# Kernel tuning notes

Measured on AMD Instinct MI355X. Metric: run time of the kernel, lower is better.

## Reference

```python
import jax, jax.numpy as jnp
import numpy as np

N_EMBD = 1024
N_HEAD = 16
HEAD_SIZE = N_EMBD // N_HEAD
EPS = 1e-5


def layer_norm(x, gamma, beta):
    mu = jnp.mean(x, axis=-1, keepdims=True)
    var = jnp.var(x, axis=-1, keepdims=True)
    return (x - mu) * jax.lax.rsqrt(var + EPS) * gamma + beta


def setup_inputs() -> dict:
    key = jax.random.key(0)
    ks = jax.random.split(key, 12)
    B, T, C, H, hs = 2, 2048, N_EMBD, N_HEAD, HEAD_SIZE
    s = lambda fan_in: 1.0 / np.sqrt(fan_in)
    return {
        "x": jax.random.normal(ks[0], (B, T, C), dtype=jnp.float32),
        "Wq": jax.random.normal(ks[1], (H, C, hs), dtype=jnp.float32) * s(C),
        "Wk": jax.random.normal(ks[2], (H, C, hs), dtype=jnp.float32) * s(C),
        "Wv": jax.random.normal(ks[3], (H, C, hs), dtype=jnp.float32) * s(C),
        "Wproj": jax.random.normal(ks[4], (C, C), dtype=jnp.float32) * s(C),
        "bproj": jax.random.normal(ks[5], (C,), dtype=jnp.float32) * 0.01,
        "g1": jnp.ones((C,), dtype=jnp.float32),
        "b1": jnp.zeros((C,), dtype=jnp.float32),
        "g2": jnp.ones((C,), dtype=jnp.float32),
        "b2": jnp.zeros((C,), dtype=jnp.float32),
        "W_ff1": jax.random.normal(ks[6], (C, 4 * C), dtype=jnp.float32) * s(C),
        "b_ff1": jax.random.normal(ks[7], (4 * C,), dtype=jnp.float32) * 0.01,
        "W_ff2": jax.random.normal(ks[8], (4 * C, C), dtype=jnp.float32) * s(4 * C),
        "b_ff2": jax.random.normal(ks[9], (C,), dtype=jnp.float32) * 0.01,
    }


def reference(x, Wq, Wk, Wv, Wproj, bproj, g1, b1, g2, b2, W_ff1, b_ff1, W_ff2, b_ff2):
    B, T, C = x.shape
    # --- LN1 + multi-head causal self-attention ---
    h = layer_norm(x, g1, b1)
    q = jnp.einsum("btc,hcd->bhtd", h, Wq)  # [B,H,T,hs]
    k = jnp.einsum("btc,hcd->bhtd", h, Wk)
    v = jnp.einsum("btc,hcd->bhtd", h, Wv)
    scale = HEAD_SIZE ** -0.5
    wei = jnp.einsum("bhtd,bhsd->bhts", q, k) * scale  # [B,H,T,T]
    mask = jnp.tril(jnp.ones((T, T), dtype=bool))
    wei = jnp.where(mask, wei, -jnp.inf)
    wei = jax.nn.softmax(wei, axis=-1)
    out = jnp.einsum("bhts,bhsd->bhtd", wei, v)  # [B,H,T,hs]
    out = out.transpose(0, 2, 1, 3).reshape(B, T, C)  # concat heads
    sa = out @ Wproj + bproj
    x = x + sa
    # --- LN2 + FFN ---
    h2 = layer_norm(x, g2, b2)
    ff = jax.nn.relu(h2 @ W_ff1 + b_ff1) @ W_ff2 + b_ff2
    return x + ff
```

## Files before the change

kernel.cpp:

```cpp
#include <hip/hip_runtime.h>
#include <hip/hip_bf16.h>

#define N_EMBD 1024
#define N_HEAD 16
#define HEADSZ 64
#define BATCH  2
#define SEQ    2048
#define ROWS   (BATCH*SEQ)

typedef __attribute__((ext_vector_type(8))) short bf16x8;
typedef __attribute__((ext_vector_type(4))) float f32x4;

__device__ __forceinline__ short f2bs(float v){
    union { __hip_bfloat16 b; short s; } u; u.b = __float2bfloat16(v); return u.s;
}
__device__ __forceinline__ short scale8th(short s){
    union { unsigned i; float f; } u; u.i = ((unsigned)(unsigned short)s) << 16;
    return f2bs(u.f * 0.125f);
}
__device__ __forceinline__ void gload16(const short* g, short* l){
    __builtin_amdgcn_global_load_lds(
        (const __attribute__((address_space(1))) unsigned int*)g,
        (__attribute__((address_space(3))) unsigned int*)l, 16, 0, 0);
}

__global__ __launch_bounds__(256) void tr_cvt(const float* __restrict__ in,
                                              short* __restrict__ out,
                                              int R, int Cc,
                                              size_t in_z, size_t out_z)
{
    __shared__ float t[32][33];
    const int tx = threadIdx.x & 31, ty = threadIdx.x >> 5;
    const int j0 = blockIdx.x * 32, i0 = blockIdx.y * 32;
    const float* ip = in + (size_t)blockIdx.z * in_z;
    short* op = out + (size_t)blockIdx.z * out_z;
#pragma unroll
    for (int p = 0; p < 4; ++p)
        t[ty + p * 8][tx] = ip[(size_t)(i0 + ty + p * 8) * Cc + j0 + tx];
    __syncthreads();
#pragma unroll
    for (int p = 0; p < 4; ++p)
        op[(size_t)(j0 + ty + p * 8) * R + i0 + tx] = f2bs(t[tx][ty + p * 8]);
}

__global__ __launch_bounds__(256) void tr3_cvt(const float* __restrict__ Wq,
                                               const float* __restrict__ Wk,
                                               const float* __restrict__ Wv,
                                               short* __restrict__ w2t)
{
    __shared__ float t[32][33];
    const int tx = threadIdx.x & 31, ty = threadIdx.x >> 5;
    const int which = blockIdx.z >> 4, head = blockIdx.z & 15;
    const int j0 = blockIdx.x * 32, i0 = blockIdx.y * 32;
    const float* ip = (which == 0 ? Wq : which == 1 ? Wk : Wv) + (size_t)head * 65536;
    short* op = w2t + (size_t)which * 1048576 + (size_t)head * 65536;
#pragma unroll
    for (int p = 0; p < 4; ++p)
        t[ty + p * 8][tx] = ip[(size_t)(i0 + ty + p * 8) * 64 + j0 + tx];
    __syncthreads();
#pragma unroll
    for (int p = 0; p < 4; ++p)
        op[(size_t)(j0 + ty + p * 8) * 1024 + i0 + tx] = f2bs(t[tx][ty + p * 8]);
}

__global__ __launch_bounds__(256) void vt_tr(const short* __restrict__ qkv,
                                             short* __restrict__ vt)
{
    __shared__ short t[64][65];
    const int tid = threadIdx.x;
    const int sr = tid >> 2, sc = (tid & 3) * 16;
    const int col0 = blockIdx.x * 64, tok0 = blockIdx.y * 64;
    const short* ip = qkv + (size_t)(tok0 + sr) * 3072 + 2048 + col0 + sc;
    bf16x8 v0 = *(const bf16x8*)ip;
    bf16x8 v1 = *(const bf16x8*)(ip + 8);
#pragma unroll
    for (int i = 0; i < 8; ++i) { t[sr][sc + i] = v0[i]; t[sr][sc + 8 + i] = v1[i]; }
    __syncthreads();
    bf16x8 a, bq;
#pragma unroll
    for (int i = 0; i < 8; ++i) { a[i] = t[sc + i][sr]; bq[i] = t[sc + 8 + i][sr]; }
    short* op = vt + (size_t)(col0 + sr) * 4096 + tok0 + sc;
    *(bf16x8*)op = a;
    *(bf16x8*)(op + 8) = bq;
}

__global__ __launch_bounds__(256) void ln_k(const float* __restrict__ x,
                                            const float* __restrict__ g,
                                            const float* __restrict__ bta,
                                            short* __restrict__ out)
{
    const int row = blockIdx.x;
    const int tid = threadIdx.x;
    const float* xr = x + (size_t)row * N_EMBD;
    float4 v = *(const float4*)(xr + tid * 4);
    float s  = v.x + v.y + v.z + v.w;
    float s2 = v.x * v.x + v.y * v.y + v.z * v.z + v.w * v.w;
#pragma unroll
    for (int off = 32; off; off >>= 1) {
        s  += __shfl_xor(s,  off, 64);
        s2 += __shfl_xor(s2, off, 64);
    }
    __shared__ float rs[4], rs2[4];
    const int wave = tid >> 6, lane = tid & 63;
    if (lane == 0) { rs[wave] = s; rs2[wave] = s2; }
    __syncthreads();
    s  = rs[0] + rs[1] + rs[2] + rs[3];
    s2 = rs2[0] + rs2[1] + rs2[2] + rs2[3];
    const float mean = s * (1.f / N_EMBD);
    const float var  = s2 * (1.f / N_EMBD) - mean * mean;
    const float rsig = rsqrtf(var + 1e-5f);
    float4 gv = *(const float4*)(g + tid * 4);
    float4 bv = *(const float4*)(bta + tid * 4);
    short4 o;
    o.x = f2bs((v.x - mean) * rsig * gv.x + bv.x);
    o.y = f2bs((v.y - mean) * rsig * gv.y + bv.y);
    o.z = f2bs((v.z - mean) * rsig * gv.z + bv.z);
    o.w = f2bs((v.w - mean) * rsig * gv.w + bv.w);
    *(short4*)(out + (size_t)row * N_EMBD + tid * 4) = o;
}

__global__ __launch_bounds__(256) void pln_fin(const float* __restrict__ p0,
                                               const float* __restrict__ p1,
                                               const float* __restrict__ bias,
                                               const float* __restrict__ x,
                                               const float* __restrict__ g,
                                               const float* __restrict__ bta,
                                               float* __restrict__ x2,
                                               short* __restrict__ h2)
{
    const int row = blockIdx.x, tid = threadIdx.x;
    const size_t base = (size_t)row * N_EMBD + tid * 4;
    float4 a  = *(const float4*)(p0 + base);
    float4 c  = *(const float4*)(p1 + base);
    float4 xx = *(const float4*)(x + base);
    float4 bb = *(const float4*)(bias + tid * 4);
    float4 v;
    v.x = a.x + c.x + xx.x + bb.x;
    v.y = a.y + c.y + xx.y + bb.y;
    v.z = a.z + c.z + xx.z + bb.z;
    v.w = a.w + c.w + xx.w + bb.w;
    *(float4*)(x2 + base) = v;
    float s  = v.x + v.y + v.z + v.w;
    float s2 = v.x * v.x + v.y * v.y + v.z * v.z + v.w * v.w;
#pragma unroll
    for (int off = 32; off; off >>= 1) {
        s  += __shfl_xor(s,  off, 64);
        s2 += __shfl_xor(s2, off, 64);
    }
    __shared__ float rs[4], rs2[4];
    const int wave = tid >> 6, lane = tid & 63;
    if (lane == 0) { rs[wave] = s; rs2[wave] = s2; }
    __syncthreads();
    s  = rs[0] + rs[1] + rs[2] + rs[3];
    s2 = rs2[0] + rs2[1] + rs2[2] + rs2[3];
    const float mean = s * (1.f / N_EMBD);
    const float var  = s2 * (1.f / N_EMBD) - mean * mean;
    const float rsig = rsqrtf(var + 1e-5f);
    float4 gv = *(const float4*)(g + tid * 4);
    float4 bv = *(const float4*)(bta + tid * 4);
    short4 o;
    o.x = f2bs((v.x - mean) * rsig * gv.x + bv.x);
    o.y = f2bs((v.y - mean) * rsig * gv.y + bv.y);
    o.z = f2bs((v.z - mean) * rsig * gv.z + bv.z);
    o.w = f2bs((v.w - mean) * rsig * gv.w + bv.w);
    *(short4*)(h2 + base) = o;
}

__global__ __launch_bounds__(256) void mfma_gemm(
    const short* __restrict__ A,
    const short* __restrict__ Bt,
    const float* __restrict__ bias,
    const float* __restrict__ resid,
    float* __restrict__ outf,
    float* __restrict__ outf2,
    short* __restrict__ outb,
    int M, int N, int K, int kz, int relu)
{
    __shared__ __align__(16) short As[3][128 * 32];
    __shared__ __align__(16) short Bs[3][128 * 32];
    const int tid  = threadIdx.x;
    const int lane = tid & 63, w = tid >> 6;
    const int quad = lane >> 4, l16 = lane & 15;
    const int row0 = blockIdx.y * 128, col0 = blockIdx.x * 128;
    const int wm = (w >> 1) * 64, wn = (w & 1) * 64;
    const int koff = blockIdx.z * kz;
    const int kend = kz ? kz : K;
    const int nk   = kend >> 5;

    f32x4 acc[4][4];
#pragma unroll
    for (int i = 0; i < 4; ++i)
#pragma unroll
        for (int j = 0; j < 4; ++j)
            acc[i][j] = f32x4{0.f, 0.f, 0.f, 0.f};

    const int c0  = w * 128 + lane;
    const int c1  = c0 + 64;
    const int ar0 = c0 >> 2, ak0 = (((c0 & 3) ^ ((ar0 >> 1) & 3))) * 8;
    const int ar1 = c1 >> 2, ak1 = (((c1 & 3) ^ ((ar1 >> 1) & 3))) * 8;
    const short* aG0 = A  + (size_t)(row0 + ar0) * K + koff + ak0;
    const short* aG1 = A  + (size_t)(row0 + ar1) * K + koff + ak1;
    const short* bG0 = Bt + (size_t)(col0 + ar0) * K + koff + ak0;
    const short* bG1 = Bt + (size_t)(col0 + ar1) * K + koff + ak1;
    const int lofs = w * 1024;

    const int gsw = (quad ^ ((l16 >> 1) & 3)) * 8;

    gload16(aG0, As[0] + lofs);
    gload16(aG1, As[0] + lofs + 512);
    gload16(bG0, Bs[0] + lofs);
    gload16(bG1, Bs[0] + lofs + 512);
    if (nk > 1) {
        gload16(aG0 + 32, As[1] + lofs);
        gload16(aG1 + 32, As[1] + lofs + 512);
        gload16(bG0 + 32, Bs[1] + lofs);
        gload16(bG1 + 32, Bs[1] + lofs + 512);
    }

    for (int k = 0; k < nk; ++k) {
        if (k + 1 < nk) asm volatile("s_waitcnt vmcnt(4)" ::: "memory");
        else            asm volatile("s_waitcnt vmcnt(0)" ::: "memory");
        __builtin_amdgcn_s_barrier();
        if (k + 2 < nk) {
            const int nb = (k + 2) % 3;
            const int ko = (k + 2) * 32;
            gload16(aG0 + ko, As[nb] + lofs);
            gload16(aG1 + ko, As[nb] + lofs + 512);
            gload16(bG0 + ko, Bs[nb] + lofs);
            gload16(bG1 + ko, Bs[nb] + lofs + 512);
        }
        const int cur = k % 3;

        bf16x8 af[4], bfr[4];
#pragma unroll
        for (int i = 0; i < 4; ++i)
            af[i]  = *(const bf16x8*)(As[cur] + (wm + i * 16 + l16) * 32 + gsw);
#pragma unroll
        for (int j = 0; j < 4; ++j)
            bfr[j] = *(const bf16x8*)(Bs[cur] + (wn + j * 16 + l16) * 32 + gsw);
#pragma unroll
        for (int i = 0; i < 4; ++i)
#pragma unroll
            for (int j = 0; j < 4; ++j)
                acc[i][j] = __builtin_amdgcn_mfma_f32_16x16x32_bf16(
                    af[i], bfr[j], acc[i][j], 0, 0, 0);
    }

    float* of = blockIdx.z ? outf2 : outf;
#pragma unroll
    for (int i = 0; i < 4; ++i) {
        const int rbase = row0 + wm + i * 16 + quad * 4;
#pragma unroll
        for (int j = 0; j < 4; ++j) {
            const int c = col0 + wn + j * 16 + l16;
            const float bv = bias ? bias[c] : 0.f;
#pragma unroll
            for (int r = 0; r < 4; ++r) {
                float v = acc[i][j][r] + bv;
                if (relu) v = fmaxf(v, 0.f);
                const size_t idx = (size_t)(rbase + r) * N + c;
                if (resid) v += resid[idx];
                if (outb) outb[idx] = f2bs(v);
                else      of[idx] = v;
            }
        }
    }
}

__global__ __launch_bounds__(256) void mfma_gemm64(
    const short* __restrict__ A,
    const short* __restrict__ Bt,
    float* __restrict__ outf,
    float* __restrict__ outf2,
    int K, int kz)
{
    __shared__ __align__(16) short As[3][64 * 32];
    __shared__ __align__(16) short Bs[3][128 * 32];
    const int tid  = threadIdx.x;
    const int lane = tid & 63, w = tid >> 6;
    const int quad = lane >> 4, l16 = lane & 15;
    const int lin  = (int)blockIdx.y * 8 + (int)blockIdx.x;
    const int swz  = (lin & 7) * 64 + (lin >> 3);
    const int col0 = (swz & 7) * 128;
    const int row0 = (swz >> 3) * 64;
    const int wr = w >> 1, wc = w & 1;
    const int koff = blockIdx.z * kz;
    const int nk   = kz >> 5;

    f32x4 acc[2][4];
#pragma unroll
    for (int i = 0; i < 2; ++i)
#pragma unroll
        for (int j = 0; j < 4; ++j)
            acc[i][j] = f32x4{0.f, 0.f, 0.f, 0.f};

    const int ia  = w * 64 + lane;
    const int ar  = ia >> 2;
    const int aak = ((ia & 3) ^ ((ar >> 1) & 3)) * 8;
    const short* aG = A + (size_t)(row0 + ar) * K + koff + aak;
    const int aofs = w * 512;
    const int c0  = w * 128 + lane;
    const int c1  = c0 + 64;
    const int br0 = c0 >> 2, bk0 = ((c0 & 3) ^ ((br0 >> 1) & 3)) * 8;
    const int br1 = c1 >> 2, bk1 = ((c1 & 3) ^ ((br1 >> 1) & 3)) * 8;
    const short* bG0 = Bt + (size_t)(col0 + br0) * K + koff + bk0;
    const short* bG1 = Bt + (size_t)(col0 + br1) * K + koff + bk1;
    const int bofs = w * 1024;

    const int gsw = (quad ^ ((l16 >> 1) & 3)) * 8;

    gload16(aG, As[0] + aofs);
    gload16(bG0, Bs[0] + bofs);
    gload16(bG1, Bs[0] + bofs + 512);
    if (nk > 1) {
        gload16(aG + 32, As[1] + aofs);
        gload16(bG0 + 32, Bs[1] + bofs);
        gload16(bG1 + 32, Bs[1] + bofs + 512);
    }

    for (int k = 0; k < nk; ++k) {
        if (k + 1 < nk) asm volatile("s_waitcnt vmcnt(3)" ::: "memory");
        else            asm volatile("s_waitcnt vmcnt(0)" ::: "memory");
        __builtin_amdgcn_s_barrier();
        if (k + 2 < nk) {
            const int nb = (k + 2) % 3;
            const int ko = (k + 2) * 32;
            gload16(aG + ko, As[nb] + aofs);
            gload16(bG0 + ko, Bs[nb] + bofs);
            gload16(bG1 + ko, Bs[nb] + bofs + 512);
        }
        const int cur = k % 3;

        bf16x8 af[2], bfr[4];
#pragma unroll
        for (int i = 0; i < 2; ++i)
            af[i]  = *(const bf16x8*)(As[cur] + (wr * 32 + i * 16 + l16) * 32 + gsw);
#pragma unroll
        for (int j = 0; j < 4; ++j)
            bfr[j] = *(const bf16x8*)(Bs[cur] + (wc * 64 + j * 16 + l16) * 32 + gsw);
#pragma unroll
        for (int i = 0; i < 2; ++i)
#pragma unroll
            for (int j = 0; j < 4; ++j)
                acc[i][j] = __builtin_amdgcn_mfma_f32_16x16x32_bf16(
                    af[i], bfr[j], acc[i][j], 0, 0, 0);
    }

    float* of = blockIdx.z ? outf2 : outf;
#pragma unroll
    for (int i = 0; i < 2; ++i) {
        const int rbase = row0 + wr * 32 + i * 16 + quad * 4;
#pragma unroll
        for (int j = 0; j < 4; ++j) {
            const int c = col0 + wc * 64 + j * 16 + l16;
#pragma unroll
            for (int r = 0; r < 4; ++r)
                of[(size_t)(rbase + r) * 1024 + c] = acc[i][j][r];
        }
    }
}

__global__ __launch_bounds__(256) void ff2_fin(const float* __restrict__ p0,
                                               const float* __restrict__ bias,
                                               const float* __restrict__ x2,
                                               float* __restrict__ out)
{
    const size_t i = ((size_t)blockIdx.x * 256 + threadIdx.x) * 4;
    float4 a = *(const float4*)(p0 + i);
    float4 b = *(const float4*)(out + i);
    float4 r = *(const float4*)(x2 + i);
    float4 bb = *(const float4*)(bias + (i & 1023));
    float4 o;
    o.x = a.x + b.x + r.x + bb.x;
    o.y = a.y + b.y + r.y + bb.y;
    o.z = a.z + b.z + r.z + bb.z;
    o.w = a.w + b.w + r.w + bb.w;
    *(float4*)(out + i) = o;
}

__global__ __launch_bounds__(256) void attn_k(const short* __restrict__ qkv,
                                              const short* __restrict__ vt,
                                              short* __restrict__ att)
{
    __shared__ __align__(16) short Ks[2][64 * 64];
    __shared__ __align__(16) short Vs[2][64 * 64];
    __shared__ __align__(16) short Ps[64 * 64];
    const int tid  = threadIdx.x;
    const int lane = tid & 63, w = tid >> 6;
    const int quad = lane >> 4, l16 = lane & 15;
    const int bh = blockIdx.y, b = bh >> 4, head = bh & 15;

    const int srow = lane >> 3;
    const int sw   = ((lane & 7) ^ srow) * 8;
    const int cidx = (quad ^ (l16 & 7)) * 8;

    const int k4 = (bh >> 3) & 3;
    int qt = (k4 & 2) ? ((int)blockIdx.x ^ 16) : (int)blockIdx.x;
    if (k4 & 1) qt = 31 - qt;
    const int t0 = qt * 64;
    const int ntiles = qt + 1;

    const short* qp = qkv + (size_t)(b * SEQ + t0 + w * 16 + l16) * 3072
                      + head * 64 + quad * 8;
    bf16x8 qf0 = *(const bf16x8*)qp;
    bf16x8 qf1 = *(const bf16x8*)(qp + 32);
#pragma unroll
    for (int i = 0; i < 8; ++i) { qf0[i] = scale8th(qf0[i]); qf1[i] = scale8th(qf1[i]); }

    float mrow = -INFINITY, lrow = 0.f;
    f32x4 O[4];
#pragma unroll
    for (int jn = 0; jn < 4; ++jn) O[jn] = f32x4{0.f, 0.f, 0.f, 0.f};

    {
        const short* kg = qkv + (size_t)(b * SEQ + w * 16 + srow) * 3072
                          + 1024 + head * 64 + sw;
        const short* vg = vt + (size_t)(head * 64 + w * 16 + srow) * 4096
                          + b * SEQ + sw;
        short* kL = Ks[0] + w * 1024;
        short* vL = Vs[0] + w * 1024;
        gload16(kg, kL); gload16(kg + (size_t)8 * 3072, kL + 512);
        gload16(vg, vL); gload16(vg + (size_t)8 * 4096, vL + 512);
    }

    for (int kt = 0; kt < ntiles; ++kt) {
        const int cur = kt & 1;
        asm volatile("s_waitcnt vmcnt(0) lgkmcnt(0)\n\ts_barrier" ::: "memory");
        if (kt + 1 < ntiles) {
            const int s1 = (kt + 1) * 64;
            const short* kg = qkv + (size_t)(b * SEQ + s1 + w * 16 + srow) * 3072
                              + 1024 + head * 64 + sw;
            const short* vg = vt + (size_t)(head * 64 + w * 16 + srow) * 4096
                              + b * SEQ + s1 + sw;
            short* kL = Ks[cur ^ 1] + w * 1024;
            short* vL = Vs[cur ^ 1] + w * 1024;
            gload16(kg, kL); gload16(kg + (size_t)8 * 3072, kL + 512);
            gload16(vg, vL); gload16(vg + (size_t)8 * 4096, vL + 512);
        }

        f32x4 S[4];
        const short* Kb = Ks[cur];
#pragma unroll
        for (int jn = 0; jn < 4; ++jn) {
            S[jn] = f32x4{0.f, 0.f, 0.f, 0.f};
            const short* kp = Kb + (jn * 16 + l16) * 64;
            bf16x8 b0 = *(const bf16x8*)(kp + cidx);
            bf16x8 b1 = *(const bf16x8*)(kp + (cidx ^ 32));
            S[jn] = __builtin_amdgcn_mfma_f32_16x16x32_bf16(b0, qf0, S[jn], 0, 0, 0);
            S[jn] = __builtin_amdgcn_mfma_f32_16x16x32_bf16(b1, qf1, S[jn], 0, 0, 0);
        }

        float Sv[4][4];
        const int qrow = t0 + w * 16 + l16;
        const int s0 = kt * 64;
#pragma unroll
        for (int jn = 0; jn < 4; ++jn)
#pragma unroll
            for (int r = 0; r < 4; ++r)
                Sv[jn][r] = S[jn][r];
        if (kt == ntiles - 1) {
#pragma unroll
            for (int jn = 0; jn < 4; ++jn)
#pragma unroll
                for (int r = 0; r < 4; ++r)
                    if (s0 + jn * 16 + quad * 4 + r > qrow) Sv[jn][r] = -INFINITY;
        }
        float tmx[4];
#pragma unroll
        for (int jn = 0; jn < 4; ++jn)
            tmx[jn] = fmaxf(fmaxf(Sv[jn][0], Sv[jn][1]), fmaxf(Sv[jn][2], Sv[jn][3]));
        float pm = fmaxf(fmaxf(tmx[0], tmx[1]), fmaxf(tmx[2], tmx[3]));
        pm = fmaxf(pm, __shfl_xor(pm, 16, 64));
        pm = fmaxf(pm, __shfl_xor(pm, 32, 64));
        const float mn    = fmaxf(mrow, pm);
        const float alpha = __expf(mrow - mn);
#pragma unroll
        for (int jn = 0; jn < 4; ++jn)
#pragma unroll
            for (int r = 0; r < 4; ++r)
                Sv[jn][r] = __expf(Sv[jn][r] - mn);
        float tsm[4];
#pragma unroll
        for (int jn = 0; jn < 4; ++jn)
            tsm[jn] = (Sv[jn][0] + Sv[jn][1]) + (Sv[jn][2] + Sv[jn][3]);
        float ps = (tsm[0] + tsm[1]) + (tsm[2] + tsm[3]);
        ps += __shfl_xor(ps, 16, 64);
        ps += __shfl_xor(ps, 32, 64);
        lrow = lrow * alpha + ps;
        mrow = mn;
#pragma unroll
        for (int r = 0; r < 4; ++r) {
            const float a = __shfl(alpha, quad * 4 + r, 64);
#pragma unroll
            for (int jn = 0; jn < 4; ++jn) O[jn][r] *= a;
        }

#pragma unroll
        for (int jn = 0; jn < 4; ++jn) {
            short4 pv;
            pv.x = f2bs(Sv[jn][0]); pv.y = f2bs(Sv[jn][1]);
            pv.z = f2bs(Sv[jn][2]); pv.w = f2bs(Sv[jn][3]);
            const int prow = w * 16 + l16;
            const int pcol = jn * 16 + quad * 4;
            const int chunk = (pcol >> 3) ^ (l16 & 7);
            *(short4*)(Ps + prow * 64 + chunk * 8 + (pcol & 7)) = pv;
        }
        asm volatile("s_waitcnt lgkmcnt(0)" ::: "memory");

        const short* pp = Ps + (w * 16 + l16) * 64;
        bf16x8 pf0 = *(const bf16x8*)(pp + cidx);
        bf16x8 pf1 = *(const bf16x8*)(pp + (cidx ^ 32));
        const short* Vb = Vs[cur];
#pragma unroll
        for (int jn = 0; jn < 4; ++jn) {
            const short* vp = Vb + (jn * 16 + l16) * 64;
            bf16x8 v0 = *(const bf16x8*)(vp + cidx);
            bf16x8 v1 = *(const bf16x8*)(vp + (cidx ^ 32));
            O[jn] = __builtin_amdgcn_mfma_f32_16x16x32_bf16(pf0, v0, O[jn], 0, 0, 0);
            O[jn] = __builtin_amdgcn_mfma_f32_16x16x32_bf16(pf1, v1, O[jn], 0, 0, 0);
        }
    }

#pragma unroll
    for (int r = 0; r < 4; ++r) {
        const float lr  = __shfl(lrow, quad * 4 + r, 64);
        const float inv = 1.f / lr;
        const size_t rowoff = (size_t)(b * SEQ + t0 + w * 16 + quad * 4 + r) * N_EMBD
                              + head * 64 + l16;
#pragma unroll
        for (int jn = 0; jn < 4; ++jn)
            att[rowoff + jn * 16] = f2bs(O[jn][r] * inv);
    }
}

extern "C" void kernel_launch(void* const* d_in, const int* in_sizes, int n_in,
                              void* d_out, int out_size, void* d_ws, size_t ws_size,
                              hipStream_t stream)
{
    const float* x     = (const float*)d_in[0];
    const float* Wq    = (const float*)d_in[1];
    const float* Wk    = (const float*)d_in[2];
    const float* Wv    = (const float*)d_in[3];
    const float* Wproj = (const float*)d_in[4];
    const float* bproj = (const float*)d_in[5];
    const float* g1    = (const float*)d_in[6];
    const float* b1    = (const float*)d_in[7];
    const float* g2    = (const float*)d_in[8];
    const float* b2    = (const float*)d_in[9];
    const float* Wff1  = (const float*)d_in[10];
    const float* bff1  = (const float*)d_in[11];
    const float* Wff2  = (const float*)d_in[12];
    const float* bff2  = (const float*)d_in[13];
    float* out = (float*)d_out;

    char* ws = (char*)d_ws;
    short* w2t  = (short*)(ws + 0);
    short* wpt  = (short*)(ws + 6291456);
    short* wf1t = (short*)(ws + 8388608);
    short* wf2t = (short*)(ws + 16777216);
    short* h    = (short*)(ws + 25165824);
    short* qkv  = (short*)(ws + 33554432);
    short* vt   = (short*)(ws + 58720256);
    short* att  = (short*)(ws + 67108864);
    float* x2   = (float*)(ws + 75497472);
    short* h2   = h;
    float* p0p  = (float*)(ws + 33554432);
    float* p1p  = (float*)(ws + 50331648);
    short* ff   = qkv;
    float* p0f  = (float*)(ws + 0);

    tr3_cvt<<<dim3(2, 32, 48),  256, 0, stream>>>(Wq, Wk, Wv, w2t);
    tr_cvt<<<dim3(32, 32, 1),  256, 0, stream>>>(Wproj, wpt,  1024, 1024, 0, 0);
    tr_cvt<<<dim3(128, 32, 1), 256, 0, stream>>>(Wff1, wf1t,  1024, 4096, 0, 0);
    tr_cvt<<<dim3(32, 128, 1), 256, 0, stream>>>(Wff2, wf2t,  4096, 1024, 0, 0);

    ln_k<<<ROWS, 256, 0, stream>>>(x, g1, b1, h);
    mfma_gemm<<<dim3(3072 / 128, ROWS / 128), 256, 0, stream>>>(
        h, w2t, nullptr, nullptr, nullptr, nullptr, qkv, ROWS, 3072, N_EMBD, 0, 0);
    vt_tr<<<dim3(16, 64), 256, 0, stream>>>(qkv, vt);
    attn_k<<<dim3(32, BATCH * N_HEAD), 256, 0, stream>>>(qkv, vt, att);
    mfma_gemm64<<<dim3(8, 64, 2), 256, 0, stream>>>(att, wpt, p0p, p1p, N_EMBD, 512);
    pln_fin<<<ROWS, 256, 0, stream>>>(p0p, p1p, bproj, x, g2, b2, x2, h2);
    mfma_gemm<<<dim3(4096 / 128, ROWS / 128), 256, 0, stream>>>(
        h2, wf1t, bff1, nullptr, nullptr, nullptr, ff, ROWS, 4096, N_EMBD, 0, 1);
    mfma_gemm64<<<dim3(8, 64, 2), 256, 0, stream>>>(ff, wf2t, p0f, out, 4096, 2048);
    ff2_fin<<<ROWS * N_EMBD / 1024, 256, 0, stream>>>(p0f, bff2, x2, out);
}
```

Before: 374.2 us.

## Use 256x256-tile 512-thread GEMM kernel for FFN1

Adds a new bf16 MFMA GEMM kernel with 256x256 output tiles, 8 waves and double-buffered LDS loads, and uses it for the FFN first layer (bias plus ReLU) in place of the 128x128 kernel. The larger tile raises arithmetic intensity and operand reuse per global load. The cost is a grid of only 256 blocks, which may underfill the GPU's compute units. The high accumulator register count and the full wait-then-barrier each k-step also limit latency hiding.

```diff
diff --git a/kernel.cpp b/kernel.cpp
--- a/kernel.cpp
+++ b/kernel.cpp
@@ -267,6 +267,94 @@
     }
 }
 
+__global__ __launch_bounds__(512, 2) void mfma_gemm256(
+    const short* __restrict__ A,
+    const short* __restrict__ Bt,
+    const float* __restrict__ bias,
+    short* __restrict__ outb,
+    int N, int K, int relu)
+{
+    __shared__ __align__(16) short As[2][256 * 32];
+    __shared__ __align__(16) short Bs[2][256 * 32];
+    const int tid  = threadIdx.x;
+    const int lane = tid & 63, w = tid >> 6;
+    const int quad = lane >> 4, l16 = lane & 15;
+    const int row0 = blockIdx.y * 256, col0 = blockIdx.x * 256;
+    const int wm = (w >> 2) * 128;
+    const int wn = (w & 3) * 64;
+    const int nk = K >> 5;
+
+    f32x4 acc[8][4];
+#pragma unroll
+    for (int i = 0; i < 8; ++i)
+#pragma unroll
+        for (int j = 0; j < 4; ++j)
+            acc[i][j] = f32x4{0.f, 0.f, 0.f, 0.f};
+
+    const int i0 = tid, i1 = tid + 512;
+    const int ar0 = i0 >> 2, ak0 = ((i0 & 3) ^ ((ar0 >> 1) & 3)) * 8;
+    const int ar1 = i1 >> 2, ak1 = ((i1 & 3) ^ ((ar1 >> 1) & 3)) * 8;
+    const short* aG0 = A  + (size_t)(row0 + ar0) * K + ak0;
+    const short* aG1 = A  + (size_t)(row0 + ar1) * K + ak1;
+    const short* bG0 = Bt + (size_t)(col0 + ar0) * K + ak0;
+    const short* bG1 = Bt + (size_t)(col0 + ar1) * K + ak1;
+    const int lofs = w * 512;
+
+    const int gsw = (quad ^ ((l16 >> 1) & 3)) * 8;
+
+    gload16(aG0, As[0] + lofs);
+    gload16(aG1, As[0] + 4096 + lofs);
+    gload16(bG0, Bs[0] + lofs);
+    gload16(bG1, Bs[0] + 4096 + lofs);
+    asm volatile("s_waitcnt vmcnt(0)" ::: "memory");
+    __builtin_amdgcn_s_barrier();
+
+    for (int k = 0; k < nk; ++k) {
+        const int cur = k & 1;
+        if (k + 1 < nk) {
+            const int ko = (k + 1) * 32;
+            const int nb = cur ^ 1;
+            gload16(aG0 + ko, As[nb] + lofs);
+            gload16(aG1 + ko, As[nb] + 4096 + lofs);
+            gload16(bG0 + ko, Bs[nb] + lofs);
+            gload16(bG1 + ko, Bs[nb] + 4096 + lofs);
+        }
+
+        bf16x8 af[8], bfr[4];
+#pragma unroll
+        for (int i = 0; i < 8; ++i)
+            af[i]  = *(const bf16x8*)(As[cur] + (wm + i * 16 + l16) * 32 + gsw);
+#pragma unroll
+        for (int j = 0; j < 4; ++j)
+            bfr[j] = *(const bf16x8*)(Bs[cur] + (wn + j * 16 + l16) * 32 + gsw);
+#pragma unroll
+        for (int i = 0; i < 8; ++i)
+#pragma unroll
+            for (int j = 0; j < 4; ++j)
+                acc[i][j] = __builtin_amdgcn_mfma_f32_16x16x32_bf16(
+                    af[i], bfr[j], acc[i][j], 0, 0, 0);
+
+        asm volatile("s_waitcnt vmcnt(0)" ::: "memory");
+        __builtin_amdgcn_s_barrier();
+    }
+
+#pragma unroll
+    for (int i = 0; i < 8; ++i) {
+        const int rbase = row0 + wm + i * 16 + quad * 4;
+#pragma unroll
+        for (int j = 0; j < 4; ++j) {
+            const int c = col0 + wn + j * 16 + l16;
+            const float bv = bias[c];
+#pragma unroll
+            for (int r = 0; r < 4; ++r) {
+                float v = acc[i][j][r] + bv;
+                if (relu) v = fmaxf(v, 0.f);
+                outb[(size_t)(rbase + r) * N + c] = f2bs(v);
+            }
+        }
+    }
+}
+
 __global__ __launch_bounds__(256) void mfma_gemm64(
     const short* __restrict__ A,
     const short* __restrict__ Bt,
@@ -581,8 +669,8 @@
     attn_k<<<dim3(32, BATCH * N_HEAD), 256, 0, stream>>>(qkv, vt, att);
     mfma_gemm64<<<dim3(8, 64, 2), 256, 0, stream>>>(att, wpt, p0p, p1p, N_EMBD, 512);
     pln_fin<<<ROWS, 256, 0, stream>>>(p0p, p1p, bproj, x, g2, b2, x2, h2);
-    mfma_gemm<<<dim3(4096 / 128, ROWS / 128), 256, 0, stream>>>(
-        h2, wf1t, bff1, nullptr, nullptr, nullptr, ff, ROWS, 4096, N_EMBD, 0, 1);
+    mfma_gemm256<<<dim3(4096 / 256, ROWS / 256), 512, 0, stream>>>(
+        h2, wf1t, bff1, ff, 4096, N_EMBD, 1);
     mfma_gemm64<<<dim3(8, 64, 2), 256, 0, stream>>>(ff, wf2t, p0f, out, 4096, 2048);
     ff2_fin<<<ROWS * N_EMBD / 1024, 256, 0, stream>>>(p0f, bff2, x2, out);
 }
```

New measurement: 374.3 us. Within noise of the previous version (+0.0%).
